# Optimization experiments

Hardware: AMD Instinct MI355X
Metric: run time of the kernel (lower is better)

Reference implementation:

```python
import jax, jax.numpy as jnp
import numpy as np

B, LQ, E = 4, 8400, 256
HEADS, LEVELS, POINTS = 8, 4, 4
HEAD_DIM = E // HEADS
SHAPES = [(80, 80), (40, 40), (20, 20), (10, 10)]  # (H, W) per level; sum HW = 8400
LV = sum(h * w for h, w in SHAPES)


def setup_inputs() -> dict:
    key = jax.random.key(0)
    ks = jax.random.split(key, 12)
    query = jax.random.normal(ks[0], (B, LQ, E), jnp.float32)
    # per-level normalized reference points in (0.1, 0.9)
    reference_points = 0.1 + 0.8 * jax.random.uniform(ks[1], (B, LQ, LEVELS, 2), jnp.float32)
    value = jax.random.normal(ks[2], (B, LV, E), jnp.float32)
    spatial_shapes = jnp.array(SHAPES, dtype=jnp.int32)
    s = 0.05
    Wv = jax.random.normal(ks[3], (E, E), jnp.float32) * s
    bv = jnp.zeros((E,), jnp.float32)
    Woff = jax.random.normal(ks[4], (E, HEADS * LEVELS * POINTS * 2), jnp.float32) * 0.01
    boff = jax.random.normal(ks[5], (HEADS * LEVELS * POINTS * 2,), jnp.float32) * 0.02
    Wattn = jax.random.normal(ks[6], (E, HEADS * LEVELS * POINTS), jnp.float32) * s
    battn = jnp.zeros((HEADS * LEVELS * POINTS,), jnp.float32)
    Wo = jax.random.normal(ks[7], (E, E), jnp.float32) * s
    bo = jnp.zeros((E,), jnp.float32)
    return dict(query=query, reference_points=reference_points, value=value,
                spatial_shapes=spatial_shapes, Wv=Wv, bv=bv, Woff=Woff, boff=boff,
                Wattn=Wattn, battn=battn, Wo=Wo, bo=bo)


def _bilinear_sample(vflat, x, y, Hl, Wl):
    # vflat: [BH, D, Hl*Wl]; x, y: [BH, N] pixel coords (align_corners=False convention)
    x0f = jnp.floor(x); y0f = jnp.floor(y)
    wx = (x - x0f)[:, None, :]; wy = (y - y0f)[:, None, :]
    x0 = x0f.astype(jnp.int32); y0 = y0f.astype(jnp.int32)

    def gather(ix, iy):
        valid = ((ix >= 0) & (ix < Wl) & (iy >= 0) & (iy < Hl)).astype(vflat.dtype)
        idx = jnp.clip(iy, 0, Hl - 1) * Wl + jnp.clip(ix, 0, Wl - 1)
        g = jnp.take_along_axis(vflat, idx[:, None, :], axis=2)  # [BH, D, N]
        return g * valid[:, None, :]

    v00 = gather(x0, y0); v01 = gather(x0 + 1, y0)
    v10 = gather(x0, y0 + 1); v11 = gather(x0 + 1, y0 + 1)
    return (v00 * (1 - wx) * (1 - wy) + v01 * wx * (1 - wy)
            + v10 * (1 - wx) * wy + v11 * wx * wy)


def _msda_forward(query, reference_points, value, spatial_shapes,
                  Wv, bv, Woff, boff, Wattn, battn, Wo, bo):
    b, lq, _ = query.shape
    v = (value @ Wv + bv).reshape(b, -1, HEADS, HEAD_DIM)
    off = (query @ Woff + boff).reshape(b, lq, HEADS, LEVELS, POINTS, 2)
    aw = (query @ Wattn + battn).reshape(b, lq, HEADS, LEVELS * POINTS)
    aw = jax.nn.softmax(aw, axis=-1).reshape(b, lq, HEADS, LEVELS, POINTS)
    # normalizer (W, H) per level
    norm = jnp.stack([spatial_shapes[:, 1], spatial_shapes[:, 0]], axis=-1).astype(query.dtype)
    # sampling locations in [0,1]: [B, Lq, H, L, P, 2]
    loc = reference_points[:, :, None, :, None, :] + off / norm[None, None, None, :, None, :]

    sampled_levels = []
    start = 0
    for lvl, (Hl, Wl) in enumerate(SHAPES):
        vl = v[:, start:start + Hl * Wl]                      # [B, Hl*Wl, H, D]
        start += Hl * Wl
        vflat = vl.transpose(0, 2, 3, 1).reshape(b * HEADS, HEAD_DIM, Hl * Wl)
        grid = loc[:, :, :, lvl]                              # [B, Lq, H, P, 2]
        grid = grid.transpose(0, 2, 1, 3, 4).reshape(b * HEADS, lq * POINTS, 2)
        g = grid * 2.0 - 1.0                                  # grid_sample convention
        x = (g[..., 0] + 1.0) * (Wl * 0.5) - 0.5
        y = (g[..., 1] + 1.0) * (Hl * 0.5) - 0.5
        s = _bilinear_sample(vflat, x, y, Hl, Wl)             # [BH, D, Lq*P]
        sampled_levels.append(s.reshape(b, HEADS, HEAD_DIM, lq, POINTS))
    sampled = jnp.stack(sampled_levels, axis=-1)              # [B, H, D, Lq, P, L]
    out = jnp.einsum('bhdqpl,bqhlp->bqhd', sampled, aw).reshape(b, lq, E)
    return out @ Wo + bo


def reference(query, reference_points, value, spatial_shapes,
              Wv, bv, Woff, boff, Wattn, battn, Wo, bo):
    return _msda_forward(query, reference_points, value, spatial_shapes,
                         Wv, bv, Woff, boff, Wattn, battn, Wo, bo)
```

## Files before the change

kernel.cpp:

```cpp
#include <hip/hip_runtime.h>
#include <math.h>

#define BB 4
#define LQ 8400
#define NH 8
#define LVTOT 8500
#define HD 32
#define PLANE_USH 544000

typedef __attribute__((ext_vector_type(8))) short short8;
typedef __attribute__((ext_vector_type(4))) float f32x4;
typedef __attribute__((ext_vector_type(2))) _Float16 half2_t;
typedef __attribute__((ext_vector_type(2))) __fp16 fp16x2_t;
typedef unsigned short ushort_t;

__device__ __forceinline__ ushort_t f2bf(float f) {
    union { float f; unsigned u; } v; v.f = f;
    unsigned r = v.u + 0x7fffu + ((v.u >> 16) & 1u);
    return (ushort_t)(r >> 16);
}
__device__ __forceinline__ float bflo(unsigned u) {
    union { unsigned u; float f; } x; x.u = u << 16; return x.f;
}
__device__ __forceinline__ float bfhi(unsigned u) {
    union { unsigned u; float f; } x; x.u = u & 0xffff0000u; return x.f;
}
__device__ __forceinline__ half2_t ash2(unsigned u) {
    union { unsigned u; half2_t h; } x; x.u = u; return x.h;
}
__device__ __forceinline__ unsigned pk2u(fp16x2_t h) {
    union { fp16x2_t h; unsigned u; } x; x.h = h; return x.u;
}

__device__ __forceinline__ void dma16(const ushort_t* g, ushort_t* l) {
    __builtin_amdgcn_global_load_lds(
        (const __attribute__((address_space(1))) void*)g,
        (__attribute__((address_space(3))) void*)l, 16, 0, 0);
}
__device__ __forceinline__ void dma16g(const void* g, void* l) {
    __builtin_amdgcn_global_load_lds(
        (const __attribute__((address_space(1))) void*)g,
        (__attribute__((address_space(3))) void*)l, 16, 0, 0);
}

__device__ __forceinline__ void lvl_decomp(int pix, int& lb, int& y, int& x,
                                           int& rowp) {
    if (pix < 6400)      { y = pix / 80;            x = pix - y * 80;  rowp = 40; lb = 0; }
    else if (pix < 8000) { int r = pix - 6400; y = r / 40; x = r - y * 40; rowp = 20; lb = 3200; }
    else if (pix < 8400) { int r = pix - 8000; y = r / 20; x = r - y * 20; rowp = 10; lb = 4000; }
    else                 { int r = pix - 8400; y = r / 10; x = r - y * 10; rowp = 5;  lb = 4200; }
}

__global__ __launch_bounds__(256) void prep_bt(
    const float* __restrict__ Wv, const float* __restrict__ Woff,
    const float* __restrict__ Wattn, const float* __restrict__ Wo,
    ushort_t* __restrict__ BT)
{
    int idx = blockIdx.x * 256 + threadIdx.x;
    int r = idx >> 8, k = idx & 255;
    float v;
    if (r < 256) v = Wv[k * 256 + r];
    else if (r < 640) {
        int n = r - 256;
        v = (n < 256) ? Woff[k * 256 + n] : Wattn[k * 128 + (n - 256)];
    } else v = Wo[k * 256 + (r - 640)];
    BT[idx] = f2bf(v);
}

__device__ __forceinline__ void gemm_core64_f32a(
    const float* __restrict__ A, const ushort_t* __restrict__ B, int M,
    int m0, int n0, float* Af, ushort_t* Bsl, f32x4 acc[2][4])
{
    const int tid  = threadIdx.x;
    const int wave = tid >> 6, lane = tid & 63;
    const int quad = lane >> 4, mr = lane & 15;
    const int wm   = (wave >> 1) * 32, wn = (wave & 1) * 64;
    const int oct  = lane >> 3;
    const int bseg = lane & 7;
    const int r4   = lane >> 4;
    const int s16  = lane & 15;

    for (int k0 = 0; k0 < 256; k0 += 64) {
        __syncthreads();
        #pragma unroll
        for (int i = 0; i < 4; i++) {
            int m  = i * 16 + wave * 4 + r4;
            int gs = s16 ^ (m & 15);
            int am = min(m0 + m, M - 1);
            dma16g((const char*)A + (size_t)am * 1024 + (size_t)(k0 + gs * 4) * 4,
                   (char*)Af + (i * 16 + wave * 4) * 256 + lane * 16);
        }
        #pragma unroll
        for (int i = 0; i < 4; i++) {
            int n  = i * 32 + wave * 8 + oct;
            int gs = bseg ^ (n & 7);
            dma16(B + (size_t)(n0 + n) * 256 + k0 + gs * 8,
                  Bsl + (i * 32 + wave * 8) * 64 + lane * 8);
        }
        __syncthreads();
        #pragma unroll
        for (int ks = 0; ks < 2; ks++) {
            short8 af[2], bf[4];
            const int ksl = ks * 4 + quad;
            #pragma unroll
            for (int i = 0; i < 2; i++) {
                int m  = wm + i * 16 + mr;
                int p0 = (ksl * 2) ^ (m & 15);
                int p1 = (ksl * 2 + 1) ^ (m & 15);
                float4 lo = *(const float4*)&Af[m * 64 + p0 * 4];
                float4 hi = *(const float4*)&Af[m * 64 + p1 * 4];
                short8 a;
                a[0] = (short)f2bf(lo.x); a[1] = (short)f2bf(lo.y);
                a[2] = (short)f2bf(lo.z); a[3] = (short)f2bf(lo.w);
                a[4] = (short)f2bf(hi.x); a[5] = (short)f2bf(hi.y);
                a[6] = (short)f2bf(hi.z); a[7] = (short)f2bf(hi.w);
                af[i] = a;
            }
            #pragma unroll
            for (int j = 0; j < 4; j++) {
                int n = wn + j * 16 + mr;
                bf[j] = *(const short8*)&Bsl[n * 64 + (ksl ^ (n & 7)) * 8];
            }
            #pragma unroll
            for (int i = 0; i < 2; i++)
                #pragma unroll
                for (int j = 0; j < 4; j++)
                    acc[i][j] = __builtin_amdgcn_mfma_f32_16x16x32_bf16(
                        af[i], bf[j], acc[i][j], 0, 0, 0);
        }
    }
}

__device__ __forceinline__ void gemm_core64(
    const ushort_t* __restrict__ A, const ushort_t* __restrict__ B, int M,
    int m0, int n0, ushort_t* Asl, ushort_t* Bsl, f32x4 acc[2][4])
{
    const int tid  = threadIdx.x;
    const int wave = tid >> 6, lane = tid & 63;
    const int quad = lane >> 4, mr = lane & 15;
    const int wm   = (wave >> 1) * 32, wn = (wave & 1) * 64;
    const int oct  = lane >> 3;
    const int bseg = lane & 7;

    for (int k0 = 0; k0 < 256; k0 += 64) {
        __syncthreads();
        #pragma unroll
        for (int i = 0; i < 2; i++) {
            int m  = i * 32 + wave * 8 + oct;
            int gs = bseg ^ (m & 7);
            int am = min(m0 + m, M - 1);
            dma16(A + (size_t)am * 256 + k0 + gs * 8,
                  Asl + (i * 32 + wave * 8) * 64 + lane * 8);
        }
        #pragma unroll
        for (int i = 0; i < 4; i++) {
            int n  = i * 32 + wave * 8 + oct;
            int gs = bseg ^ (n & 7);
            dma16(B + (size_t)(n0 + n) * 256 + k0 + gs * 8,
                  Bsl + (i * 32 + wave * 8) * 64 + lane * 8);
        }
        __syncthreads();
        #pragma unroll
        for (int ks = 0; ks < 2; ks++) {
            short8 af[2], bf[4];
            const int ksl = ks * 4 + quad;
            #pragma unroll
            for (int i = 0; i < 2; i++) {
                int m = wm + i * 16 + mr;
                af[i] = *(const short8*)&Asl[m * 64 + (ksl ^ (m & 7)) * 8];
            }
            #pragma unroll
            for (int j = 0; j < 4; j++) {
                int n = wn + j * 16 + mr;
                bf[j] = *(const short8*)&Bsl[n * 64 + (ksl ^ (n & 7)) * 8];
            }
            #pragma unroll
            for (int i = 0; i < 2; i++)
                #pragma unroll
                for (int j = 0; j < 4; j++)
                    acc[i][j] = __builtin_amdgcn_mfma_f32_16x16x32_bf16(
                        af[i], bf[j], acc[i][j], 0, 0, 0);
        }
    }
}

__global__ __launch_bounds__(256, 4) void gemm_fused(
    const float* __restrict__ Av, const float* __restrict__ Aq,
    const ushort_t* __restrict__ BT,
    const float* __restrict__ bv, const float* __restrict__ boff,
    const float* __restrict__ battn,
    ushort_t* __restrict__ vperm, ushort_t* __restrict__ off_b,
    ushort_t* __restrict__ awl_b)
{
    __shared__ ushort_t smem[16384];
    float*    Af  = (float*)smem;
    ushort_t* Bsl = smem + 8192;

    const int bid = blockIdx.x;
    int mode, m0, n0, M;
    const float* A;
    const ushort_t* B;
    if (bid < 1064) { mode = 0; m0 = (bid >> 1) * 64; n0 = (bid & 1) * 128;
                      A = Av; B = BT; M = 34000; }
    else { int b2 = bid - 1064;
           mode = 1; m0 = (b2 / 3) * 64; n0 = (b2 % 3) * 128;
           A = Aq; B = BT + 65536; M = 33600; }

    f32x4 acc[2][4];
    #pragma unroll
    for (int i = 0; i < 2; i++)
        #pragma unroll
        for (int j = 0; j < 4; j++) acc[i][j] = (f32x4){0.f, 0.f, 0.f, 0.f};

    gemm_core64_f32a(A, B, M, m0, n0, Af, Bsl, acc);

    const int tid  = threadIdx.x;
    const int wave = tid >> 6, lane = tid & 63;
    const int quad = lane >> 4, mr = lane & 15;
    const int wm   = (wave >> 1) * 32, wn = (wave & 1) * 64;

    __syncthreads();
    #pragma unroll
    for (int i = 0; i < 2; i++) {
        #pragma unroll
        for (int j = 0; j < 4; j++) {
            const int lc = wn + j * 16 + mr;
            const int c  = n0 + lc;
            const float bias = (mode == 0) ? bv[c]
                              : (c < 256 ? boff[c] : battn[c - 256]);
            #pragma unroll
            for (int reg = 0; reg < 4; reg++) {
                const int rl = wm + i * 16 + quad * 4 + reg;
                float val = acc[i][j][reg] + bias;
                ushort_t u;
                if (mode == 0) { union { _Float16 h; ushort_t u; } cv;
                                 cv.h = (_Float16)val; u = cv.u; }
                else u = f2bf(val);
                smem[rl * 128 + (lc ^ ((rl & 3) << 3))] = u;
            }
        }
    }
    __syncthreads();

    if (mode == 1) {
        #pragma unroll
        for (int k = 0; k < 4; k++) {
            int sid = k * 256 + tid;
            int rl = sid >> 4, cc = (sid & 15) * 8;
            int row = m0 + rl;
            if (row >= M) continue;
            uint4 v = *(const uint4*)&smem[rl * 128 + (cc ^ ((rl & 3) << 3))];
            if (n0 < 256) *(uint4*)&off_b[(size_t)row * 256 + n0 + cc] = v;
            else          *(uint4*)&awl_b[(size_t)row * 128 + cc] = v;
        }
    } else {
        const int hb = n0 >> 5;
        #pragma unroll
        for (int k = 0; k < 8; k++) {
            int sid = k * 256 + tid;
            int unit = sid >> 5;
            if (unit >= 63) continue;
            int sub = sid & 31;
            int hh = sub >> 3, q = sub & 7;
            int copy = (unit >= 32) ? 1 : 0;
            int t = copy ? ((unit - 32) * 2 + 1) : (unit * 2);
            int row = m0 + t;
            if (row + 1 >= 34000) continue;
            int b = row / LVTOT, pix = row - b * LVTOT;
            int lb, y, x, rowp;
            lvl_decomp(pix, lb, y, x, rowp);
            if (copy && x >= 2 * rowp - 1) continue;
            int p = x >> 1;
            int pidx = copy * 4250 + lb + y * rowp + p;
            int h = hb + hh;
            uint2 a  = *(const uint2*)&smem[t * 128 +
                          ((hh * 32 + q * 4) ^ ((t & 3) << 3))];
            uint2 b2 = *(const uint2*)&smem[(t + 1) * 128 +
                          ((hh * 32 + q * 4) ^ (((t + 1) & 3) << 3))];
            uint4 o;
            o.x = (a.x & 0xffffu) | (b2.x << 16);
            o.y = (a.x >> 16)     | (b2.x & 0xffff0000u);
            o.z = (a.y & 0xffffu) | (b2.y << 16);
            o.w = (a.y >> 16)     | (b2.y & 0xffff0000u);
            *(uint4*)((char*)(vperm + (size_t)(b * NH + h) * PLANE_USH)
                      + (size_t)pidx * 128 + q * 16) = o;
        }
        {
            int pixsel = tid >> 7;
            int rem = tid & 127;
            int hh = rem >> 5, d = rem & 31;
            int t = pixsel ? 63 : 0;
            int row = m0 + t;
            if (row < 34000) {
                int b = row / LVTOT, pix = row - b * LVTOT;
                int lb, y, x, rowp;
                lvl_decomp(pix, lb, y, x, rowp);
                bool doit; int p, slot;
                if (!pixsel) { doit = (x >= 2);            p = (x - 2) >> 1; slot = 1; }
                else         { doit = (x < 2 * rowp - 1);  p = (x - 1) >> 1; slot = 0; }
                if (doit) {
                    int pidx = 4250 + lb + y * rowp + p;
                    int h = hb + hh;
                    vperm[(size_t)(b * NH + h) * PLANE_USH
                          + (size_t)pidx * 64 + d * 2 + slot] =
                        smem[t * 128 + ((hh * 32 + d) ^ ((t & 3) << 3))];
                }
            }
        }
    }
}

__global__ __launch_bounds__(256, 4) void gemm_out(
    const ushort_t* __restrict__ A, const ushort_t* __restrict__ BT,
    const float* __restrict__ bo, float* __restrict__ out)
{
    __shared__ ushort_t smem[12288];
    ushort_t* Asl = smem;
    ushort_t* Bsl = smem + 4096;

    const int m0 = (blockIdx.x >> 1) * 64;
    const int n0 = (blockIdx.x & 1) * 128;
    const int M = 33600;

    f32x4 acc[2][4];
    #pragma unroll
    for (int i = 0; i < 2; i++)
        #pragma unroll
        for (int j = 0; j < 4; j++) acc[i][j] = (f32x4){0.f, 0.f, 0.f, 0.f};

    gemm_core64(A, BT, M, m0, n0, Asl, Bsl, acc);

    const int tid  = threadIdx.x;
    const int wave = tid >> 6, lane = tid & 63;
    const int quad = lane >> 4, mr = lane & 15;
    const int half = wave >> 1;
    const int wn   = (wave & 1) * 64;
    float* fsm = (float*)smem;

    #pragma unroll
    for (int i = 0; i < 2; i++) {
        __syncthreads();
        #pragma unroll
        for (int j = 0; j < 4; j++) {
            const int lc = wn + j * 16 + mr;
            const float bias = bo[n0 + lc];
            #pragma unroll
            for (int reg = 0; reg < 4; reg++) {
                const int rloc = half * 16 + quad * 4 + reg;
                const int cs = lc ^ (quad << 4);
                fsm[rloc * 128 + cs] = acc[i][j][reg] + bias;
            }
        }
        __syncthreads();
        #pragma unroll
        for (int k = 0; k < 4; k++) {
            int sid = k * 256 + tid;
            int rloc = sid >> 5, cw = (sid & 31) * 4;
            int row = m0 + (rloc >> 4) * 32 + i * 16 + (rloc & 15);
            if (row >= M) continue;
            int q2 = (rloc >> 2) & 3;
            float4 v = *(const float4*)&fsm[rloc * 128 + (cw ^ (q2 << 4))];
            *(float4*)&out[(size_t)row * 256 + n0 + cw] = v;
        }
    }
}

__global__ __launch_bounds__(256) void msda_sample(
    const ushort_t* __restrict__ vperm, const ushort_t* __restrict__ off,
    const ushort_t* __restrict__ awl, const float* __restrict__ refp,
    ushort_t* __restrict__ sampled)
{
    __shared__ int4 s_wi[16 * 33];

    const int tid = threadIdx.x;
    const int bid = blockIdx.x;
    const int h   = bid & 7;
    const int r   = bid >> 3;
    const int b   = r / 263;
    const int c   = r - b * 263;
    const int q0b = c * 32;
    const size_t bq0 = (size_t)b * LQ + q0b;

    const int Hs[4]    = {80, 40, 20, 10};
    const int pbase[4] = {0, 3200, 4000, 4200};

    #pragma unroll
    for (int it = 0; it < 2; it++) {
        const int s  = it * 256 + tid;
        const int ql = s >> 4, lp = s & 15;
        const int l  = lp >> 2;
        const int qv = (q0b + ql < LQ) ? ql : 0;
        const size_t bq = bq0 + qv;
        const int Wl = Hs[l];

        unsigned od = *(const unsigned*)(off + bq * 256 + h * 32 + lp * 2);
        float ox = bflo(od), oy = bfhi(od);
        float lgt = bflo((unsigned)awl[bq * 128 + h * 16 + lp]);
        float e = __expf(lgt);
        float sum = e;
        sum += __shfl_xor(sum, 1, 16);
        sum += __shfl_xor(sum, 2, 16);
        sum += __shfl_xor(sum, 4, 16);
        sum += __shfl_xor(sum, 8, 16);
        float aw = e * __builtin_amdgcn_rcpf(sum);

        float2 rp = *(const float2*)(refp + bq * 8 + l * 2);
        float x = rp.x * (float)Wl + ox - 0.5f;
        float y = rp.y * (float)Wl + oy - 0.5f;
        float x0f = floorf(x), y0f = floorf(y);
        float wx = x - x0f, wy = y - y0f;
        int x0 = (int)x0f, y0 = (int)y0f;
        float hx0 = ((x0 >= 0) & (x0 < Wl)) ? (1.f - wx) : 0.f;
        float hx1 = ((x0 + 1 >= 0) & (x0 + 1 < Wl)) ? wx : 0.f;
        float vy0w = ((y0 >= 0) & (y0 < Wl)) ? (1.f - wy) * aw : 0.f;
        float vy1w = ((y0 + 1 >= 0) & (y0 + 1 < Wl)) ? wy * aw : 0.f;
        int px = min(max(x0, 0), Wl - 2);
        float pl, pr;
        if (x0 < px)      { pl = hx1; pr = 0.f; }
        else if (x0 > px) { pl = 0.f; pr = hx0; }
        else              { pl = hx0; pr = hx1; }
        int cy0 = min(max(y0, 0), Wl - 1);
        int cy1 = min(max(y0 + 1, 0), Wl - 1);
        const int copy = px & 1;
        const int p    = copy ? ((px - 1) >> 1) : (px >> 1);
        const int rowp = Wl >> 1;
        const int cb   = copy * 4250 + pbase[l] + p;
        const int otop = (cb + cy0 * rowp) << 7;
        const int obot = (cb + cy1 * rowp) << 7;
        unsigned wt = pk2u(__builtin_amdgcn_cvt_pkrtz(pl * vy0w, pr * vy0w));
        unsigned wb = pk2u(__builtin_amdgcn_cvt_pkrtz(pl * vy1w, pr * vy1w));
        s_wi[lp * 33 + ql] = make_int4((int)wt, (int)wb, otop, obot);
    }
    __syncthreads();

    const int ql  = tid >> 3;
    const int l8  = tid & 7;
    const int dby = l8 * 16;

    if (q0b + ql < LQ) {
        const char* plane = (const char*)(vperm + (size_t)(b * NH + h) * PLANE_USH);
        float a0 = 0.f, a1 = 0.f, a2 = 0.f, a3 = 0.f;
        #pragma unroll
        for (int pt = 0; pt < 16; pt++) {
            int4 wi = s_wi[pt * 33 + ql];
            uint4 vt = *(const uint4*)(plane + (unsigned)(wi.z + dby));
            uint4 vb = *(const uint4*)(plane + (unsigned)(wi.w + dby));
            half2_t wt = ash2((unsigned)wi.x);
            half2_t wb = ash2((unsigned)wi.y);
            a0 = __builtin_amdgcn_fdot2(wt, ash2(vt.x), a0, false);
            a0 = __builtin_amdgcn_fdot2(wb, ash2(vb.x), a0, false);
            a1 = __builtin_amdgcn_fdot2(wt, ash2(vt.y), a1, false);
            a1 = __builtin_amdgcn_fdot2(wb, ash2(vb.y), a1, false);
            a2 = __builtin_amdgcn_fdot2(wt, ash2(vt.z), a2, false);
            a2 = __builtin_amdgcn_fdot2(wb, ash2(vb.z), a2, false);
            a3 = __builtin_amdgcn_fdot2(wt, ash2(vt.w), a3, false);
            a3 = __builtin_amdgcn_fdot2(wb, ash2(vb.w), a3, false);
        }
        const size_t bq = bq0 + ql;
        ushort4 o;
        o.x = f2bf(a0); o.y = f2bf(a1);
        o.z = f2bf(a2); o.w = f2bf(a3);
        *(ushort4*)(sampled + bq * 256 + h * 32 + l8 * 4) = o;
    }
}

extern "C" void kernel_launch(void* const* d_in, const int* in_sizes, int n_in,
                              void* d_out, int out_size, void* d_ws, size_t ws_size,
                              hipStream_t stream) {
    const float* query = (const float*)d_in[0];
    const float* refp  = (const float*)d_in[1];
    const float* value = (const float*)d_in[2];
    const float* Wv    = (const float*)d_in[4];
    const float* bv    = (const float*)d_in[5];
    const float* Woff  = (const float*)d_in[6];
    const float* boff  = (const float*)d_in[7];
    const float* Wattn = (const float*)d_in[8];
    const float* battn = (const float*)d_in[9];
    const float* Wo    = (const float*)d_in[10];
    const float* bo    = (const float*)d_in[11];
    float* out = (float*)d_out;

    ushort_t* ws = (ushort_t*)d_ws;
    ushort_t* off_b   = ws;
    ushort_t* awl_b   = off_b + 8601600;
    ushort_t* vperm_b = awl_b + 4300800;
    ushort_t* BT      = vperm_b + 17408000;
    ushort_t* sampled_b = BT + 229376;

    prep_bt<<<dim3(896), 256, 0, stream>>>(Wv, Woff, Wattn, Wo, BT);

    gemm_fused<<<dim3(1064 + 1575), 256, 0, stream>>>(
        value, query, BT, bv, boff, battn, vperm_b, off_b, awl_b);

    msda_sample<<<dim3(8 * 4 * 263), 256, 0, stream>>>(
        vperm_b, off_b, awl_b, refp, sampled_b);

    gemm_out<<<dim3(1050), 256, 0, stream>>>(
        sampled_b, BT + 163840, bo, out);
}
```

Measured before the change: 207.1 us.

## Widen fused projection GEMM tiles to full 256 columns to reuse A loads

The fused value/offset/attention projection GEMM now uses 64x256 tiles for the value and offset projections and 64x128 tiles for the attention-weight projection, instead of 64x128 tiles throughout. Each fp32 A row block is therefore loaded and converted to bf16 once per projection rather than two or three times. This cuts redundant global A traffic and conversion work. In exchange, each block uses more accumulator registers and LDS, and the launch bound drops from 4 to 3 blocks per CU with fewer total blocks.

```diff
diff --git a/kernel.cpp b/kernel.cpp
--- a/kernel.cpp
+++ b/kernel.cpp
@@ -67,14 +67,15 @@
     BT[idx] = f2bf(v);
 }
 
-__device__ __forceinline__ void gemm_core64_f32a(
+template<int NF>
+__device__ __forceinline__ void gcore_f32a(
     const float* __restrict__ A, const ushort_t* __restrict__ B, int M,
-    int m0, int n0, float* Af, ushort_t* Bsl, f32x4 acc[2][4])
+    int m0, float* Af, ushort_t* Bsl, f32x4 acc[2][NF])
 {
     const int tid  = threadIdx.x;
     const int wave = tid >> 6, lane = tid & 63;
     const int quad = lane >> 4, mr = lane & 15;
-    const int wm   = (wave >> 1) * 32, wn = (wave & 1) * 64;
+    const int wm   = (wave >> 1) * 32, wn = (wave & 1) * (NF * 16);
     const int oct  = lane >> 3;
     const int bseg = lane & 7;
     const int r4   = lane >> 4;
@@ -91,16 +92,16 @@
                    (char*)Af + (i * 16 + wave * 4) * 256 + lane * 16);
         }
         #pragma unroll
-        for (int i = 0; i < 4; i++) {
+        for (int i = 0; i < NF; i++) {
             int n  = i * 32 + wave * 8 + oct;
             int gs = bseg ^ (n & 7);
-            dma16(B + (size_t)(n0 + n) * 256 + k0 + gs * 8,
+            dma16(B + (size_t)n * 256 + k0 + gs * 8,
                   Bsl + (i * 32 + wave * 8) * 64 + lane * 8);
         }
         __syncthreads();
         #pragma unroll
         for (int ks = 0; ks < 2; ks++) {
-            short8 af[2], bf[4];
+            short8 af[2], bf[NF];
             const int ksl = ks * 4 + quad;
             #pragma unroll
             for (int i = 0; i < 2; i++) {
@@ -117,14 +118,14 @@
                 af[i] = a;
             }
             #pragma unroll
-            for (int j = 0; j < 4; j++) {
+            for (int j = 0; j < NF; j++) {
                 int n = wn + j * 16 + mr;
                 bf[j] = *(const short8*)&Bsl[n * 64 + (ksl ^ (n & 7)) * 8];
             }
             #pragma unroll
             for (int i = 0; i < 2; i++)
                 #pragma unroll
-                for (int j = 0; j < 4; j++)
+                for (int j = 0; j < NF; j++)
                     acc[i][j] = __builtin_amdgcn_mfma_f32_16x16x32_bf16(
                         af[i], bf[j], acc[i][j], 0, 0, 0);
         }
@@ -184,7 +185,7 @@
     }
 }
 
-__global__ __launch_bounds__(256, 4) void gemm_fused(
+__global__ __launch_bounds__(256, 3) void gemm_fused(
     const float* __restrict__ Av, const float* __restrict__ Aq,
     const ushort_t* __restrict__ BT,
     const float* __restrict__ bv, const float* __restrict__ boff,
@@ -192,75 +193,48 @@
     ushort_t* __restrict__ vperm, ushort_t* __restrict__ off_b,
     ushort_t* __restrict__ awl_b)
 {
-    __shared__ ushort_t smem[16384];
+    __shared__ ushort_t smem[24576];
     float*    Af  = (float*)smem;
     ushort_t* Bsl = smem + 8192;
 
-    const int bid = blockIdx.x;
-    int mode, m0, n0, M;
-    const float* A;
-    const ushort_t* B;
-    if (bid < 1064) { mode = 0; m0 = (bid >> 1) * 64; n0 = (bid & 1) * 128;
-                      A = Av; B = BT; M = 34000; }
-    else { int b2 = bid - 1064;
-           mode = 1; m0 = (b2 / 3) * 64; n0 = (b2 % 3) * 128;
-           A = Aq; B = BT + 65536; M = 33600; }
-
-    f32x4 acc[2][4];
-    #pragma unroll
-    for (int i = 0; i < 2; i++)
-        #pragma unroll
-        for (int j = 0; j < 4; j++) acc[i][j] = (f32x4){0.f, 0.f, 0.f, 0.f};
-
-    gemm_core64_f32a(A, B, M, m0, n0, Af, Bsl, acc);
-
+    const int bid  = blockIdx.x;
     const int tid  = threadIdx.x;
     const int wave = tid >> 6, lane = tid & 63;
     const int quad = lane >> 4, mr = lane & 15;
-    const int wm   = (wave >> 1) * 32, wn = (wave & 1) * 64;
-
-    __syncthreads();
-    #pragma unroll
-    for (int i = 0; i < 2; i++) {
-        #pragma unroll
-        for (int j = 0; j < 4; j++) {
-            const int lc = wn + j * 16 + mr;
-            const int c  = n0 + lc;
-            const float bias = (mode == 0) ? bv[c]
-                              : (c < 256 ? boff[c] : battn[c - 256]);
-            #pragma unroll
-            for (int reg = 0; reg < 4; reg++) {
-                const int rl = wm + i * 16 + quad * 4 + reg;
-                float val = acc[i][j][reg] + bias;
-                ushort_t u;
-                if (mode == 0) { union { _Float16 h; ushort_t u; } cv;
-                                 cv.h = (_Float16)val; u = cv.u; }
-                else u = f2bf(val);
-                smem[rl * 128 + (lc ^ ((rl & 3) << 3))] = u;
-            }
-        }
-    }
-    __syncthreads();
-
-    if (mode == 1) {
-        #pragma unroll
-        for (int k = 0; k < 4; k++) {
+    const int wm   = (wave >> 1) * 32;
+
+    if (bid < 532) {
+        const int m0 = bid * 64;
+        f32x4 acc[2][8];
+        #pragma unroll
+        for (int i = 0; i < 2; i++)
+            #pragma unroll
+            for (int j = 0; j < 8; j++) acc[i][j] = (f32x4){0.f, 0.f, 0.f, 0.f};
+        gcore_f32a<8>(Av, BT, 34000, m0, Af, Bsl, acc);
+
+        const int wn = (wave & 1) * 128;
+        __syncthreads();
+        #pragma unroll
+        for (int i = 0; i < 2; i++) {
+            #pragma unroll
+            for (int j = 0; j < 8; j++) {
+                const int lc = wn + j * 16 + mr;
+                const float bias = bv[lc];
+                #pragma unroll
+                for (int reg = 0; reg < 4; reg++) {
+                    const int rl = wm + i * 16 + quad * 4 + reg;
+                    union { _Float16 h; ushort_t u; } cv;
+                    cv.h = (_Float16)(acc[i][j][reg] + bias);
+                    smem[rl * 256 + (lc ^ ((rl & 3) << 3))] = cv.u;
+                }
+            }
+        }
+        __syncthreads();
+        for (int k = 0; k < 16; k++) {
             int sid = k * 256 + tid;
-            int rl = sid >> 4, cc = (sid & 15) * 8;
-            int row = m0 + rl;
-            if (row >= M) continue;
-            uint4 v = *(const uint4*)&smem[rl * 128 + (cc ^ ((rl & 3) << 3))];
-            if (n0 < 256) *(uint4*)&off_b[(size_t)row * 256 + n0 + cc] = v;
-            else          *(uint4*)&awl_b[(size_t)row * 128 + cc] = v;
-        }
-    } else {
-        const int hb = n0 >> 5;
-        #pragma unroll
-        for (int k = 0; k < 8; k++) {
-            int sid = k * 256 + tid;
-            int unit = sid >> 5;
+            int unit = sid >> 6;
             if (unit >= 63) continue;
-            int sub = sid & 31;
+            int sub = sid & 63;
             int hh = sub >> 3, q = sub & 7;
             int copy = (unit >= 32) ? 1 : 0;
             int t = copy ? ((unit - 32) * 2 + 1) : (unit * 2);
@@ -272,22 +246,22 @@
             if (copy && x >= 2 * rowp - 1) continue;
             int p = x >> 1;
             int pidx = copy * 4250 + lb + y * rowp + p;
-            int h = hb + hh;
-            uint2 a  = *(const uint2*)&smem[t * 128 +
+            uint2 a  = *(const uint2*)&smem[t * 256 +
                           ((hh * 32 + q * 4) ^ ((t & 3) << 3))];
-            uint2 b2 = *(const uint2*)&smem[(t + 1) * 128 +
+            uint2 b2 = *(const uint2*)&smem[(t + 1) * 256 +
                           ((hh * 32 + q * 4) ^ (((t + 1) & 3) << 3))];
             uint4 o;
             o.x = (a.x & 0xffffu) | (b2.x << 16);
             o.y = (a.x >> 16)     | (b2.x & 0xffff0000u);
             o.z = (a.y & 0xffffu) | (b2.y << 16);
             o.w = (a.y >> 16)     | (b2.y & 0xffff0000u);
-            *(uint4*)((char*)(vperm + (size_t)(b * NH + h) * PLANE_USH)
+            *(uint4*)((char*)(vperm + (size_t)(b * NH + hh) * PLANE_USH)
                       + (size_t)pidx * 128 + q * 16) = o;
         }
-        {
-            int pixsel = tid >> 7;
-            int rem = tid & 127;
+        for (int it = 0; it < 2; it++) {
+            int s = it * 256 + tid;
+            int pixsel = s >> 8;
+            int rem = s & 255;
             int hh = rem >> 5, d = rem & 31;
             int t = pixsel ? 63 : 0;
             int row = m0 + t;
@@ -300,12 +274,81 @@
                 else         { doit = (x < 2 * rowp - 1);  p = (x - 1) >> 1; slot = 0; }
                 if (doit) {
                     int pidx = 4250 + lb + y * rowp + p;
-                    int h = hb + hh;
-                    vperm[(size_t)(b * NH + h) * PLANE_USH
+                    vperm[(size_t)(b * NH + hh) * PLANE_USH
                           + (size_t)pidx * 64 + d * 2 + slot] =
-                        smem[t * 128 + ((hh * 32 + d) ^ ((t & 3) << 3))];
+                        smem[t * 256 + ((hh * 32 + d) ^ ((t & 3) << 3))];
                 }
             }
+        }
+    } else if (bid < 1057) {
+        const int m0 = (bid - 532) * 64;
+        f32x4 acc[2][8];
+        #pragma unroll
+        for (int i = 0; i < 2; i++)
+            #pragma unroll
+            for (int j = 0; j < 8; j++) acc[i][j] = (f32x4){0.f, 0.f, 0.f, 0.f};
+        gcore_f32a<8>(Aq, BT + 65536, 33600, m0, Af, Bsl, acc);
+
+        const int wn = (wave & 1) * 128;
+        __syncthreads();
+        #pragma unroll
+        for (int i = 0; i < 2; i++) {
+            #pragma unroll
+            for (int j = 0; j < 8; j++) {
+                const int lc = wn + j * 16 + mr;
+                const float bias = boff[lc];
+                #pragma unroll
+                for (int reg = 0; reg < 4; reg++) {
+                    const int rl = wm + i * 16 + quad * 4 + reg;
+                    smem[rl * 256 + (lc ^ ((rl & 3) << 3))] =
+                        f2bf(acc[i][j][reg] + bias);
+                }
+            }
+        }
+        __syncthreads();
+        #pragma unroll
+        for (int k = 0; k < 8; k++) {
+            int sid = k * 256 + tid;
+            int rl = sid >> 5, cc = (sid & 31) * 8;
+            int row = m0 + rl;
+            if (row >= 33600) continue;
+            uint4 v = *(const uint4*)&smem[rl * 256 + (cc ^ ((rl & 3) << 3))];
+            *(uint4*)&off_b[(size_t)row * 256 + cc] = v;
+        }
+    } else {
+        const int m0 = (bid - 1057) * 64;
+        f32x4 acc[2][4];
+        #pragma unroll
+        for (int i = 0; i < 2; i++)
+            #pragma unroll
+            for (int j = 0; j < 4; j++) acc[i][j] = (f32x4){0.f, 0.f, 0.f, 0.f};
+        gcore_f32a<4>(Aq, BT + 131072, 33600, m0, Af, Bsl, acc);
+
+        const int wn = (wave & 1) * 64;
+        __syncthreads();
+        #pragma unroll
+        for (int i = 0; i < 2; i++) {
+            #pragma unroll
+            for (int j = 0; j < 4; j++) {
+                const int lc = wn + j * 16 + mr;
+                const float bias = battn[lc];
+                #pragma unroll
+                for (int reg = 0; reg < 4; reg++) {
+                    const int rl = wm + i * 16 + quad * 4 + reg;
+                    smem[rl * 128 + (lc ^ ((rl & 3) << 3))] =
+                        f2bf(acc[i][j][reg] + bias);
+                }
+            }
+        }
+        __syncthreads();
+        #pragma unroll
+        for (int k = 0; k < 4; k++) {
+            int sid = k * 256 + tid;
+            int rl = sid >> 4, cc = (sid & 15) * 8;
+            int row = m0 + rl;
+            if (row >= 33600) continue;
+            uint4 v = *(const uint4*)&smem[rl * 128 + (cc ^ ((rl & 3) << 3))];
+            *(uint4*)&awl_b[(size_t)row * 128 + cc] = v;
         }
     }
 }
@@ -489,7 +532,7 @@
 
     prep_bt<<<dim3(896), 256, 0, stream>>>(Wv, Woff, Wattn, Wo, BT);
 
-    gemm_fused<<<dim3(1064 + 1575), 256, 0, stream>>>(
+    gemm_fused<<<dim3(1582), 256, 0, stream>>>(
         value, query, BT, bv, boff, battn, vperm_b, off_b, awl_b);
 
     msda_sample<<<dim3(8 * 4 * 263), 256, 0, stream>>>(
```

New measurement: 203.6 us. About the same (-1.7%).
